# Kernel optimization log

Hardware: AMD Instinct MI355X
Metric: run time of the kernel (lower is better)

Reference implementation:

```python
import jax, jax.numpy as jnp
import numpy as np

C = 256          # channels
KS = 7           # kernel_size
G = 256          # groups (defaults to channels)
HID = C // 4     # hidden = channels // reduction
BN_EPS = 1e-5


def setup_inputs() -> dict:
    key = jax.random.key(0)
    ks = jax.random.split(key, 4)
    B, H, W = 4, 64, 64
    return {
        "x": jax.random.normal(ks[0], (B, C, H, W), jnp.float32),
        "reduce_w": jax.random.normal(ks[1], (HID, C), jnp.float32) / np.float32(np.sqrt(C)),
        "bn_gamma": jnp.ones((HID,), jnp.float32),
        "bn_beta": jnp.zeros((HID,), jnp.float32),
        "bn_mean": jnp.zeros((HID,), jnp.float32),
        "bn_var": jnp.ones((HID,), jnp.float32),
        "kproj_w": jax.random.normal(ks[2], (KS * KS * G, HID), jnp.float32) / np.float32(np.sqrt(HID)),
        "kproj_b": jnp.zeros((KS * KS * G,), jnp.float32),
    }


def _kernels(x, reduce_w, bn_gamma, bn_beta, bn_mean, bn_var, kproj_w, kproj_b):
    # 1x1 conv -> BN (eval mode) -> ReLU -> 1x1 conv, then per-pixel L2 kernel norm
    B, _, H, W = x.shape
    h = jnp.einsum('bchw,oc->bohw', x, reduce_w)
    inv = bn_gamma / jnp.sqrt(bn_var + BN_EPS)
    h = h * inv[None, :, None, None] + (bn_beta - bn_mean * inv)[None, :, None, None]
    h = jax.nn.relu(h)
    ker = jnp.einsum('bchw,oc->bohw', h, kproj_w) + kproj_b[None, :, None, None]
    ker = ker.reshape(B, G, KS * KS, H, W)           # (B, G, k*k, H, W)
    # kernel_norm == 'l2': zero-mean + unit L2 norm over the k*k taps
    ker = ker - ker.mean(axis=2, keepdims=True)
    denom = jnp.maximum(jnp.sqrt(jnp.sum(ker * ker, axis=2, keepdims=True)), 1e-6)
    return ker / denom


def reference(x, reduce_w, bn_gamma, bn_beta, bn_mean, bn_var, kproj_w, kproj_b):
    # get_kernels is under @torch.no_grad() in the original -> stop_gradient
    ker = jax.lax.stop_gradient(
        _kernels(x, reduce_w, bn_gamma, bn_beta, bn_mean, bn_var, kproj_w, kproj_b))
    B, Cc, H, W = x.shape
    pad = KS // 2
    gc = Cc // G  # = 1 for depthwise involution
    xp = jnp.pad(x, ((0, 0), (0, 0), (pad, pad), (pad, pad)))
    xg = xp.reshape(B, G, gc, H + 2 * pad, W + 2 * pad)
    # fused unfold-multiply-accumulate over the k*k taps (no (B,C,k,k,H,W) tensor)
    out = jnp.zeros((B, G, gc, H, W), x.dtype)
    for t in range(KS * KS):
        i, j = divmod(t, KS)
        out = out + xg[:, :, :, i:i + H, j:j + W] * ker[:, :, t][:, :, None]
    return out.reshape(B, Cc, H, W)
```

## Files before the change

### kernel.cpp

```cpp
#include <hip/hip_runtime.h>


#define C_    256
#define HID_  64
#define KS_   7
#define KK_   49
#define G_    256
#define H_    64
#define W_    64
#define HW_   4096
#define BN_EPS 1e-5f

typedef __attribute__((ext_vector_type(8))) short bf16x8;
typedef __attribute__((ext_vector_type(4))) float f32x4;

__device__ __forceinline__ ushort f2bf(float f) {
    unsigned u = __float_as_uint(f);
    return (ushort)((u + 0x7fffu + ((u >> 16) & 1u)) >> 16);
}
__device__ __forceinline__ float bf2f(ushort s) {
    return __uint_as_float((unsigned)s << 16);
}

__global__ __launch_bounds__(256) void prep_kernel(
    const float* __restrict__ kw, const float* __restrict__ kb,
    const float* __restrict__ reduce_w,
    const float* __restrict__ bn_gamma, const float* __restrict__ bn_beta,
    const float* __restrict__ bn_mean, const float* __restrict__ bn_var,
    ushort* __restrict__ kwb, float* __restrict__ rwT, float* __restrict__ betp,
    float* __restrict__ kbp)
{
    const int bid = blockIdx.x;
    if (bid < 256) {
        int idx  = bid * 256 + threadIdx.x;
        int base = idx * 16;
        int g    = base >> 12;
        int rem  = base & 4095;
        int t    = rem >> 6;
        int k0   = rem & 63;
        if (t == 49 || t == 50) return;
        union { ushort s[16]; uint4 v[2]; } u;
        if (t < KK_) {
            const float* src = kw + ((size_t)(g * KK_ + t)) * HID_ + k0;
            #pragma unroll
            for (int i = 0; i < 16; ++i) u.s[i] = f2bf(src[i]);
        } else {
            #pragma unroll
            for (int i = 0; i < 16; ++i) u.s[i] = 0;
        }
        uint4* dst = (uint4*)(kwb + base);
        dst[0] = u.v[0];
        dst[1] = u.v[1];
    } else if (bid == 256) {
        int k = threadIdx.x;
        #pragma unroll 1
        for (int o = 0; o < HID_; ++o) {
            float inv = bn_gamma[o] * rsqrtf(bn_var[o] + BN_EPS);
            rwT[k * HID_ + o] = reduce_w[o * C_ + k] * inv;
        }
        if (k < HID_) {
            float inv = bn_gamma[k] * rsqrtf(bn_var[k] + BN_EPS);
            betp[k] = bn_beta[k] - bn_mean[k] * inv;
        }
    } else if (bid == 257) {
        for (int i = threadIdx.x; i < G_ * 64; i += 256) {
            int g = i >> 6, t = i & 63;
            if (t == 49) continue;
            kbp[i] = (t < KK_) ? kb[g * KK_ + t] : 0.f;
        }
    } else {
        const int g = bid - 258;
        __shared__ float part[4][64];
        const int k  = threadIdx.x & 63;
        const int pr = threadIdx.x >> 6;
        const int t0 = pr * 13;
        const int t1 = (t0 + 13 < KK_) ? t0 + 13 : KK_;
        float s = 0.f;
        for (int t = t0; t < t1; ++t)
            s += kw[((size_t)(g * KK_ + t)) * HID_ + k];
        part[pr][k] = s;
        __syncthreads();
        if (threadIdx.x < 64) {
            float u = part[0][k] + part[1][k] + part[2][k] + part[3][k];
            ushort uh = f2bf(u);
            ushort ul = f2bf(u - bf2f(uh));
            kwb[(size_t)g * 4096 + 49 * 64 + k] = uh;
            kwb[(size_t)g * 4096 + 50 * 64 + k] = ul;
            float bs = (k < KK_) ? kb[g * KK_ + k] : 0.f;
            #pragma unroll
            for (int off = 32; off >= 1; off >>= 1) bs += __shfl_xor(bs, off);
            if (k == 0) kbp[g * 64 + 49] = bs;
        }
    }
}

__global__ __launch_bounds__(256) void hv1_kernel(
    const float* __restrict__ x, const float* __restrict__ rwT,
    float* __restrict__ hvp, int npx)
{
    const int lane = threadIdx.x & 63;
    const int wq   = __builtin_amdgcn_readfirstlane(threadIdx.x >> 6);
    const int kq   = blockIdx.y;
    const int p    = blockIdx.x * 64 + lane;
    const int b    = p >> 12;
    const int hw   = p & 4095;

    float acc[16];
    #pragma unroll
    for (int j = 0; j < 16; ++j) acc[j] = 0.f;

    const float* xp = x + ((size_t)b * C_ + kq * 64) * HW_ + hw;
    const float* rw = rwT + (kq * 64) * HID_ + wq * 16;
    #pragma unroll 8
    for (int kk = 0; kk < 64; ++kk) {
        float xk = xp[(size_t)kk * HW_];
        #pragma unroll
        for (int j = 0; j < 16; ++j) acc[j] = fmaf(xk, rw[kk * HID_ + j], acc[j]);
    }
    float* dst = hvp + ((size_t)(kq * 64 + wq * 16)) * npx + p;
    #pragma unroll
    for (int j = 0; j < 16; ++j) dst[(size_t)j * npx] = acc[j];
}

__global__ __launch_bounds__(256) void hv2_kernel(
    const float* __restrict__ hvp, const float* __restrict__ betp,
    ushort* __restrict__ hv, int npx)
{
    const int p  = blockIdx.x * 256 + threadIdx.x;
    const int o0 = blockIdx.y * 4;
    ushort s[4];
    #pragma unroll
    for (int j = 0; j < 4; ++j) {
        float v = 0.f;
        #pragma unroll
        for (int kq = 0; kq < 4; ++kq)
            v += hvp[(size_t)(kq * 64 + o0 + j) * npx + p];
        s[j] = f2bf(fmaxf(v + betp[o0 + j], 0.f));
    }
    uint2 w;
    w.x = (uint)s[0] | ((uint)s[1] << 16);
    w.y = (uint)s[2] | ((uint)s[3] << 16);
    *(uint2*)(hv + (size_t)p * HID_ + o0) = w;
}

__global__ __launch_bounds__(256) void invol_main(
    const float* __restrict__ x, const ushort* __restrict__ hv,
    const ushort* __restrict__ kwb, const float* __restrict__ kbp,
    float* __restrict__ out)
{
    __shared__ float x_s[38][72];
    __shared__ float hs_s[38][64];
    __shared__ float vs_s[32][64];

    const int tid  = threadIdx.x;
    const int lane = tid & 63;
    const int wave = __builtin_amdgcn_readfirstlane(tid >> 6);
    const int bg   = blockIdx.x;
    const int b    = bg >> 8;
    const int g    = bg & 255;
    const int y0   = blockIdx.y << 5;
    const int l15  = lane & 15;
    const int l4   = lane >> 4;

    const float* xg = x + (size_t)bg * HW_;
    for (int idx = tid; idx < 38 * 72; idx += 256) {
        int r = idx / 72, c = idx - r * 72;
        int yy = y0 - 3 + r;
        int cc = c - 3;
        bool v = ((unsigned)yy < 64u) && ((unsigned)cc < 64u);
        x_s[r][c] = v ? xg[yy * 64 + cc] : 0.f;
    }

    bf16x8 ka[2][4];
    const char* kwg = (const char*)kwb + (size_t)g * 8192;
    #pragma unroll
    for (int ks = 0; ks < 2; ++ks)
        #pragma unroll
        for (int tm = 0; tm < 4; ++tm) {
            int byte = (tm * 16 + l15) * 128 + ks * 64 + l4 * 16;
            ka[ks][tm] = *(const bf16x8*)(kwg + byte);
        }
    f32x4 kv[4];
    #pragma unroll
    for (int tm = 0; tm < 4; ++tm)
        kv[tm] = *(const f32x4*)(kbp + g * 64 + tm * 16 + l4 * 4);

    int po[3][4];
    #pragma unroll
    for (int tm = 0; tm < 3; ++tm)
        #pragma unroll
        for (int r = 0; r < 4; ++r) {
            int t = tm * 16 + l4 * 4 + r;
            int i = (t * 147) >> 10;
            int j = t - i * 7;
            po[tm][r] = i * 72 + l15 + j;
        }
    const int po48 = 6 * 72 + l15 + 6;

    __syncthreads();

    if (tid < 152) {
        int r  = tid >> 2;
        int c0 = (tid & 3) << 4;
        float s = 0.f;
        #pragma unroll
        for (int j = 0; j < 7; ++j) s += x_s[r][c0 + j];
        hs_s[r][c0] = s;
        #pragma unroll
        for (int c = 1; c < 16; ++c) {
            s += x_s[r][c0 + c + 6] - x_s[r][c0 + c - 1];
            hs_s[r][c0 + c] = s;
        }
    }
    __syncthreads();
    {
        int c   = tid & 63;
        int ry0 = (tid >> 6) << 3;
        float s = 0.f;
        #pragma unroll
        for (int i = 0; i < 7; ++i) s += hs_s[ry0 + i][c];
        vs_s[ry0][c] = s;
        #pragma unroll
        for (int k = 1; k < 8; ++k) {
            s += hs_s[ry0 + k + 6][c] - hs_s[ry0 + k - 1][c];
            vs_s[ry0 + k][c] = s;
        }
    }
    __syncthreads();

    const int rowpix0 = (b << 12) + (y0 << 6);

    #pragma unroll 2
    for (int rr = 0; rr < 8; ++rr) {
        const int ry = rr * 4 + wave;
        const int y  = y0 + ry;

        bf16x8 hb[2][4];
        #pragma unroll
        for (int ks = 0; ks < 2; ++ks)
            #pragma unroll
            for (int pn = 0; pn < 4; ++pn) {
                const char* p = (const char*)(hv +
                    (size_t)(rowpix0 + (ry << 6) + pn * 16 + l15) * HID_)
                    + ks * 64 + l4 * 16;
                hb[ks][pn] = *(const bf16x8*)p;
            }

        f32x4 acc[4][4];
        #pragma unroll
        for (int tm = 0; tm < 4; ++tm)
            #pragma unroll
            for (int pn = 0; pn < 4; ++pn) acc[tm][pn] = kv[tm];
        #pragma unroll
        for (int ks = 0; ks < 2; ++ks)
            #pragma unroll
            for (int tm = 0; tm < 4; ++tm)
                #pragma unroll
                for (int pn = 0; pn < 4; ++pn)
                    acc[tm][pn] = __builtin_amdgcn_mfma_f32_16x16x32_bf16(
                        ka[ks][tm], hb[ks][pn], acc[tm][pn], 0, 0, 0);

        float m_all[4], inv_[4];
        #pragma unroll
        for (int pn = 0; pn < 4; ++pn) {
            float ssq = 0.f;
            #pragma unroll
            for (int tm = 0; tm < 3; ++tm)
                #pragma unroll
                for (int r = 0; r < 4; ++r) {
                    float e = acc[tm][pn][r];
                    ssq = fmaf(e, e, ssq);
                }
            float e48 = acc[3][pn][0];
            ssq = fmaf(e48, e48, ssq);
            ssq += __shfl_xor(ssq, 16);
            ssq += __shfl_xor(ssq, 32);
            float mr = acc[3][pn][1] + acc[3][pn][2];
            float m  = __shfl(mr, l15) * (1.f / 49.f);
            float ss = fmaxf(ssq - 49.f * m * m, 0.f);
            m_all[pn] = m;
            inv_[pn]  = 1.f / fmaxf(sqrtf(ss), 1e-6f);
        }

        float kx[4] = {0.f, 0.f, 0.f, 0.f};
        const float* xrow = &x_s[ry][0];
        #pragma unroll
        for (int tm = 0; tm < 3; ++tm)
            #pragma unroll
            for (int r = 0; r < 4; ++r) {
                const float* bp = xrow + po[tm][r];
                #pragma unroll
                for (int pn = 0; pn < 4; ++pn)
                    kx[pn] = fmaf(acc[tm][pn][r], bp[pn * 16], kx[pn]);
            }
        {
            const float* bp = xrow + po48;
            #pragma unroll
            for (int pn = 0; pn < 4; ++pn)
                kx[pn] = fmaf(acc[3][pn][0], bp[pn * 16], kx[pn]);
        }
        float k2[4];
        #pragma unroll
        for (int pn = 0; pn < 4; ++pn) {
            float v = kx[pn];
            v += __shfl_xor(v, 16);
            v += __shfl_xor(v, 32);
            k2[pn] = v;
        }
        float k2s = (l4 == 0) ? k2[0] : (l4 == 1) ? k2[1] : (l4 == 2) ? k2[2] : k2[3];
        float ms  = (l4 == 0) ? m_all[0] : (l4 == 1) ? m_all[1] : (l4 == 2) ? m_all[2] : m_all[3];
        float is  = (l4 == 0) ? inv_[0] : (l4 == 1) ? inv_[1] : (l4 == 2) ? inv_[2] : inv_[3];
        float x2  = vs_s[ry][lane];
        out[(size_t)bg * HW_ + (y << 6) + lane] = (k2s - ms * x2) * is;
    }
}

__global__ __launch_bounds__(256) void hv_kernel(
    const float* __restrict__ x, const float* __restrict__ rwT,
    const float* __restrict__ betp, ushort* __restrict__ hv)
{
    const int lane = threadIdx.x & 63;
    const int q    = __builtin_amdgcn_readfirstlane(threadIdx.x >> 6);
    const int p    = blockIdx.x * 64 + lane;
    const int b    = p >> 12;
    const int hw   = p & 4095;
    float acc[16];
    #pragma unroll
    for (int j = 0; j < 16; ++j) acc[j] = betp[q * 16 + j];
    const float* xp = x + (size_t)b * C_ * HW_ + hw;
    #pragma unroll 8
    for (int k = 0; k < C_; ++k) {
        float xk = xp[(size_t)k * HW_];
        const float* rw = rwT + k * HID_ + q * 16;
        #pragma unroll
        for (int j = 0; j < 16; ++j) acc[j] = fmaf(xk, rw[j], acc[j]);
    }
    union { ushort s[16]; uint4 v[2]; } u;
    #pragma unroll
    for (int j = 0; j < 16; ++j) u.s[j] = f2bf(fmaxf(acc[j], 0.f));
    uint4* dst = (uint4*)(hv + (size_t)p * HID_ + q * 16);
    dst[0] = u.v[0];
    dst[1] = u.v[1];
}

__global__ __launch_bounds__(256) void invol_fallback(
    const float* __restrict__ x, const float* __restrict__ reduce_w,
    const float* __restrict__ bn_gamma, const float* __restrict__ bn_beta,
    const float* __restrict__ bn_mean, const float* __restrict__ bn_var,
    const float* __restrict__ kw, const float* __restrict__ kb,
    float* __restrict__ out)
{
    __shared__ float rwT[C_][HID_ + 4];
    __shared__ float bns[HID_];
    __shared__ float bnb[HID_];
    const int tid = threadIdx.x;
    const int b  = blockIdx.z;
    const int g0 = blockIdx.y * 32;
    const int p  = blockIdx.x * 256 + tid;
    const int py = p >> 6;
    const int px = p & 63;
    #pragma unroll 1
    for (int o = 0; o < HID_; ++o) rwT[tid][o] = reduce_w[o * C_ + tid];
    if (tid < HID_) {
        float inv = bn_gamma[tid] * rsqrtf(bn_var[tid] + BN_EPS);
        bns[tid] = inv;
        bnb[tid] = bn_beta[tid] - bn_mean[tid] * inv;
    }
    __syncthreads();
    float hvv[HID_];
    #pragma unroll
    for (int o = 0; o < HID_; ++o) hvv[o] = 0.f;
    const float* xb = x + (size_t)b * C_ * HW_ + p;
    #pragma unroll 4
    for (int k = 0; k < C_; ++k) {
        float xk = xb[(size_t)k * HW_];
        const float4* wr = (const float4*)&rwT[k][0];
        #pragma unroll
        for (int o4 = 0; o4 < HID_ / 4; ++o4) {
            float4 w = wr[o4];
            hvv[o4*4+0] = fmaf(xk, w.x, hvv[o4*4+0]);
            hvv[o4*4+1] = fmaf(xk, w.y, hvv[o4*4+1]);
            hvv[o4*4+2] = fmaf(xk, w.z, hvv[o4*4+2]);
            hvv[o4*4+3] = fmaf(xk, w.w, hvv[o4*4+3]);
        }
    }
    #pragma unroll
    for (int o = 0; o < HID_; ++o) hvv[o] = fmaxf(fmaf(hvv[o], bns[o], bnb[o]), 0.f);
    #pragma unroll 1
    for (int gi = 0; gi < 32; ++gi) {
        const int g = g0 + gi;
        const float* kwg = kw + (size_t)g * KK_ * HID_;
        float acc[KK_];
        #pragma unroll
        for (int t = 0; t < KK_; ++t) {
            float a = kb[g * KK_ + t];
            const float4* row = (const float4*)(kwg + t * HID_);
            #pragma unroll
            for (int k4 = 0; k4 < HID_ / 4; ++k4) {
                float4 w = row[k4];
                a = fmaf(w.x, hvv[k4*4+0], a);
                a = fmaf(w.y, hvv[k4*4+1], a);
                a = fmaf(w.z, hvv[k4*4+2], a);
                a = fmaf(w.w, hvv[k4*4+3], a);
            }
            acc[t] = a;
        }
        float mean = 0.f;
        #pragma unroll
        for (int t = 0; t < KK_; ++t) mean += acc[t];
        mean *= (1.f / 49.f);
        float ss = 0.f;
        #pragma unroll
        for (int t = 0; t < KK_; ++t) { acc[t] -= mean; ss = fmaf(acc[t], acc[t], ss); }
        float inv = 1.f / fmaxf(sqrtf(ss), 1e-6f);
        const float* xg = x + ((size_t)(b * G_ + g)) * HW_;
        float oacc = 0.f;
        #pragma unroll
        for (int i = 0; i < KS_; ++i) {
            int yv = py + i - 3;
            bool rok = ((unsigned)yv < (unsigned)H_);
            const float* xrow = xg + yv * W_;
            #pragma unroll
            for (int j = 0; j < KS_; ++j) {
                int xx = px + j - 3;
                bool ok = rok && ((unsigned)xx < (unsigned)W_);
                float v = ok ? xrow[xx] : 0.f;
                oacc = fmaf(v, acc[i*7+j], oacc);
            }
        }
        out[((size_t)(b * G_ + g)) * HW_ + p] = oacc * inv;
    }
}

extern "C" void kernel_launch(void* const* d_in, const int* in_sizes, int n_in,
                              void* d_out, int out_size, void* d_ws, size_t ws_size,
                              hipStream_t stream) {
    const float* x        = (const float*)d_in[0];
    const float* reduce_w = (const float*)d_in[1];
    const float* bn_gamma = (const float*)d_in[2];
    const float* bn_beta  = (const float*)d_in[3];
    const float* bn_mean  = (const float*)d_in[4];
    const float* bn_var   = (const float*)d_in[5];
    const float* kproj_w  = (const float*)d_in[6];
    const float* kproj_b  = (const float*)d_in[7];
    float* out = (float*)d_out;
    const int B   = in_sizes[0] / (C_ * HW_);
    const int npx = B * HW_;

    size_t kwb_off = 0;
    size_t kwb_sz  = (size_t)G_ * 64 * 64 * 2;
    size_t kbp_off = kwb_off + kwb_sz;
    size_t kbp_sz  = (size_t)G_ * 64 * 4;
    size_t rwt_off = kbp_off + kbp_sz;
    size_t rwt_sz  = (size_t)C_ * HID_ * 4;
    size_t bet_off = rwt_off + rwt_sz;
    size_t bet_sz  = 256;
    size_t hv_off  = bet_off + bet_sz;
    size_t hv_sz   = (size_t)npx * HID_ * 2;
    size_t hvp_off = hv_off + hv_sz;
    size_t hvp_sz  = (size_t)4 * HID_ * npx * 4;
    size_t need2   = hvp_off;
    size_t need    = hvp_off + hvp_sz;

    if (ws_size < need2) {
        dim3 grid(HW_ / 256, G_ / 32, B);
        invol_fallback<<<grid, 256, 0, stream>>>(x, reduce_w, bn_gamma, bn_beta,
                                                 bn_mean, bn_var, kproj_w, kproj_b, out);
        return;
    }

    ushort* kwb  = (ushort*)((char*)d_ws + kwb_off);
    float*  kbp  = (float*)((char*)d_ws + kbp_off);
    float*  rwT  = (float*)((char*)d_ws + rwt_off);
    float*  betp = (float*)((char*)d_ws + bet_off);
    ushort* hv   = (ushort*)((char*)d_ws + hv_off);
    float*  hvp  = (float*)((char*)d_ws + hvp_off);

    prep_kernel<<<dim3(258 + G_), 256, 0, stream>>>(kproj_w, kproj_b, reduce_w,
                                                    bn_gamma, bn_beta, bn_mean, bn_var,
                                                    kwb, rwT, betp, kbp);
    if (ws_size >= need) {
        hv1_kernel<<<dim3(npx / 64, 4), 256, 0, stream>>>(x, rwT, hvp, npx);
        hv2_kernel<<<dim3(npx / 256, 16), 256, 0, stream>>>(hvp, betp, hv, npx);
    } else {
        hv_kernel<<<dim3(npx / 64), 256, 0, stream>>>(x, rwT, betp, hv);
    }
    invol_main<<<dim3(B * G_, 2), 256, 0, stream>>>(x, hv, kwb, kbp, out);
}
```

Baseline: 148.8 us.

## Double-buffer hv loads, replicate mean taps, and merge cross-lane reductions

The main loop in the involution kernel now uses two register buffers for the bf16 hidden vectors, so loads for the next row pair are issued while the current rows run their MFMAs and epilogue. The sum-row weights and bias are replicated into all four padded tap slots, so every lane group holds the mean term without the extra __shfl broadcast. The per-pixel sum-of-squares and kx reductions use a select-and-exchange pattern that needs fewer shuffles. The box-sum prologue caches shared-memory values in registers. This raises register pressure and leaves more code written as macros.

Result: slower. 154.7 us, median of 2 (+4.0%).

```diff
diff --git a/kernel.cpp b/kernel.cpp
--- a/kernel.cpp
+++ b/kernel.cpp
@@ -20,6 +20,20 @@
 }
 __device__ __forceinline__ float bf2f(ushort s) {
     return __uint_as_float((unsigned)s << 16);
+}
+__device__ __forceinline__ float sel4(int l4, float a0, float a1, float a2, float a3) {
+    float lo = (l4 & 1) ? a1 : a0;
+    float hi = (l4 & 1) ? a3 : a2;
+    return (l4 & 2) ? hi : lo;
+}
+__device__ __forceinline__ float reduce4(int l4, float v0, float v1, float v2, float v3) {
+    float own = sel4(l4, v0, v1, v2, v3);
+    float x1  = sel4(l4, v1, v0, v3, v2);
+    float x2_ = sel4(l4, v2, v3, v0, v1);
+    float x3  = sel4(l4, v3, v2, v1, v0);
+    float s1  = own + __shfl_xor(x1, 16);
+    float s1c = x2_ + __shfl_xor(x3, 16);
+    return s1 + __shfl_xor(s1c, 32);
 }
 
 __global__ __launch_bounds__(256) void prep_kernel(
@@ -38,7 +52,7 @@
         int rem  = base & 4095;
         int t    = rem >> 6;
         int k0   = rem & 63;
-        if (t == 49 || t == 50) return;
+        if (t >= 49 && ((t - 49) & 3) <= 1) return;
         union { ushort s[16]; uint4 v[2]; } u;
         if (t < KK_) {
             const float* src = kw + ((size_t)(g * KK_ + t)) * HID_ + k0;
@@ -65,7 +79,7 @@
     } else if (bid == 257) {
         for (int i = threadIdx.x; i < G_ * 64; i += 256) {
             int g = i >> 6, t = i & 63;
-            if (t == 49) continue;
+            if (t >= 49 && ((t - 49) & 3) == 0) continue;
             kbp[i] = (t < KK_) ? kb[g * KK_ + t] : 0.f;
         }
     } else {
@@ -84,12 +98,18 @@
             float u = part[0][k] + part[1][k] + part[2][k] + part[3][k];
             ushort uh = f2bf(u);
             ushort ul = f2bf(u - bf2f(uh));
-            kwb[(size_t)g * 4096 + 49 * 64 + k] = uh;
-            kwb[(size_t)g * 4096 + 50 * 64 + k] = ul;
+            #pragma unroll
+            for (int rr = 0; rr < 4; ++rr) {
+                kwb[(size_t)g * 4096 + (49 + rr * 4) * 64 + k] = uh;
+                kwb[(size_t)g * 4096 + (50 + rr * 4) * 64 + k] = ul;
+            }
             float bs = (k < KK_) ? kb[g * KK_ + k] : 0.f;
             #pragma unroll
             for (int off = 32; off >= 1; off >>= 1) bs += __shfl_xor(bs, off);
-            if (k == 0) kbp[g * 64 + 49] = bs;
+            if (k == 0) {
+                #pragma unroll
+                for (int rr = 0; rr < 4; ++rr) kbp[g * 64 + 49 + rr * 4] = bs;
+            }
         }
     }
 }
@@ -202,13 +222,14 @@
     if (tid < 152) {
         int r  = tid >> 2;
         int c0 = (tid & 3) << 4;
-        float s = 0.f;
-        #pragma unroll
-        for (int j = 0; j < 7; ++j) s += x_s[r][c0 + j];
+        float v[22];
+        #pragma unroll
+        for (int i = 0; i < 22; ++i) v[i] = x_s[r][c0 + i];
+        float s = v[0] + v[1] + v[2] + v[3] + v[4] + v[5] + v[6];
         hs_s[r][c0] = s;
         #pragma unroll
         for (int c = 1; c < 16; ++c) {
-            s += x_s[r][c0 + c + 6] - x_s[r][c0 + c - 1];
+            s += v[c + 6] - v[c - 1];
             hs_s[r][c0 + c] = s;
         }
     }
@@ -216,13 +237,14 @@
     {
         int c   = tid & 63;
         int ry0 = (tid >> 6) << 3;
-        float s = 0.f;
-        #pragma unroll
-        for (int i = 0; i < 7; ++i) s += hs_s[ry0 + i][c];
+        float h[14];
+        #pragma unroll
+        for (int i = 0; i < 14; ++i) h[i] = hs_s[ry0 + i][c];
+        float s = h[0] + h[1] + h[2] + h[3] + h[4] + h[5] + h[6];
         vs_s[ry0][c] = s;
         #pragma unroll
         for (int k = 1; k < 8; ++k) {
-            s += hs_s[ry0 + k + 6][c] - hs_s[ry0 + k - 1][c];
+            s += h[k + 6] - h[k - 1];
             vs_s[ry0 + k][c] = s;
         }
     }
@@ -230,89 +252,89 @@
 
     const int rowpix0 = (b << 12) + (y0 << 6);
 
-    #pragma unroll 2
-    for (int rr = 0; rr < 8; ++rr) {
-        const int ry = rr * 4 + wave;
-        const int y  = y0 + ry;
-
-        bf16x8 hb[2][4];
-        #pragma unroll
-        for (int ks = 0; ks < 2; ++ks)
-            #pragma unroll
-            for (int pn = 0; pn < 4; ++pn) {
-                const char* p = (const char*)(hv +
-                    (size_t)(rowpix0 + (ry << 6) + pn * 16 + l15) * HID_)
-                    + ks * 64 + l4 * 16;
-                hb[ks][pn] = *(const bf16x8*)p;
-            }
-
-        f32x4 acc[4][4];
-        #pragma unroll
-        for (int tm = 0; tm < 4; ++tm)
-            #pragma unroll
-            for (int pn = 0; pn < 4; ++pn) acc[tm][pn] = kv[tm];
-        #pragma unroll
-        for (int ks = 0; ks < 2; ++ks)
-            #pragma unroll
-            for (int tm = 0; tm < 4; ++tm)
-                #pragma unroll
-                for (int pn = 0; pn < 4; ++pn)
-                    acc[tm][pn] = __builtin_amdgcn_mfma_f32_16x16x32_bf16(
-                        ka[ks][tm], hb[ks][pn], acc[tm][pn], 0, 0, 0);
-
-        float m_all[4], inv_[4];
-        #pragma unroll
-        for (int pn = 0; pn < 4; ++pn) {
-            float ssq = 0.f;
-            #pragma unroll
-            for (int tm = 0; tm < 3; ++tm)
-                #pragma unroll
-                for (int r = 0; r < 4; ++r) {
-                    float e = acc[tm][pn][r];
-                    ssq = fmaf(e, e, ssq);
-                }
-            float e48 = acc[3][pn][0];
-            ssq = fmaf(e48, e48, ssq);
-            ssq += __shfl_xor(ssq, 16);
-            ssq += __shfl_xor(ssq, 32);
-            float mr = acc[3][pn][1] + acc[3][pn][2];
-            float m  = __shfl(mr, l15) * (1.f / 49.f);
-            float ss = fmaxf(ssq - 49.f * m * m, 0.f);
-            m_all[pn] = m;
-            inv_[pn]  = 1.f / fmaxf(sqrtf(ss), 1e-6f);
-        }
-
-        float kx[4] = {0.f, 0.f, 0.f, 0.f};
-        const float* xrow = &x_s[ry][0];
-        #pragma unroll
-        for (int tm = 0; tm < 3; ++tm)
-            #pragma unroll
-            for (int r = 0; r < 4; ++r) {
-                const float* bp = xrow + po[tm][r];
-                #pragma unroll
-                for (int pn = 0; pn < 4; ++pn)
-                    kx[pn] = fmaf(acc[tm][pn][r], bp[pn * 16], kx[pn]);
-            }
-        {
-            const float* bp = xrow + po48;
-            #pragma unroll
-            for (int pn = 0; pn < 4; ++pn)
-                kx[pn] = fmaf(acc[3][pn][0], bp[pn * 16], kx[pn]);
-        }
-        float k2[4];
-        #pragma unroll
-        for (int pn = 0; pn < 4; ++pn) {
-            float v = kx[pn];
-            v += __shfl_xor(v, 16);
-            v += __shfl_xor(v, 32);
-            k2[pn] = v;
-        }
-        float k2s = (l4 == 0) ? k2[0] : (l4 == 1) ? k2[1] : (l4 == 2) ? k2[2] : k2[3];
-        float ms  = (l4 == 0) ? m_all[0] : (l4 == 1) ? m_all[1] : (l4 == 2) ? m_all[2] : m_all[3];
-        float is  = (l4 == 0) ? inv_[0] : (l4 == 1) ? inv_[1] : (l4 == 2) ? inv_[2] : inv_[3];
-        float x2  = vs_s[ry][lane];
-        out[(size_t)bg * HW_ + (y << 6) + lane] = (k2s - ms * x2) * is;
-    }
+#define LOAD_HB(HB, RY) do {                                               \
+    const int ryl_ = (RY);                                                 \
+    _Pragma("unroll")                                                      \
+    for (int ks = 0; ks < 2; ++ks)                                         \
+        _Pragma("unroll")                                                  \
+        for (int pn = 0; pn < 4; ++pn) {                                   \
+            const char* p_ = (const char*)(hv +                            \
+                (size_t)(rowpix0 + (ryl_ << 6) + pn * 16 + l15) * HID_)    \
+                + ks * 64 + l4 * 16;                                       \
+            HB[ks][pn] = *(const bf16x8*)p_;                               \
+        }                                                                  \
+} while (0)
+
+#define BODY(HB, RY) do {                                                  \
+    const int ry_ = (RY);                                                  \
+    f32x4 acc[4][4];                                                       \
+    _Pragma("unroll")                                                      \
+    for (int tm = 0; tm < 4; ++tm)                                         \
+        _Pragma("unroll")                                                  \
+        for (int pn = 0; pn < 4; ++pn) acc[tm][pn] = kv[tm];               \
+    _Pragma("unroll")                                                      \
+    for (int ks = 0; ks < 2; ++ks)                                         \
+        _Pragma("unroll")                                                  \
+        for (int tm = 0; tm < 4; ++tm)                                     \
+            _Pragma("unroll")                                              \
+            for (int pn = 0; pn < 4; ++pn)                                 \
+                acc[tm][pn] = __builtin_amdgcn_mfma_f32_16x16x32_bf16(     \
+                    ka[ks][tm], HB[ks][pn], acc[tm][pn], 0, 0, 0);         \
+    float ssqp[4], mp[4], kxp[4];                                          \
+    const float* xrow = &x_s[ry_][0];                                      \
+    _Pragma("unroll")                                                      \
+    for (int pn = 0; pn < 4; ++pn) {                                       \
+        float ssq = 0.f;                                                   \
+        _Pragma("unroll")                                                  \
+        for (int tm = 0; tm < 3; ++tm)                                     \
+            _Pragma("unroll")                                              \
+            for (int r = 0; r < 4; ++r) {                                  \
+                float e = acc[tm][pn][r];                                  \
+                ssq = fmaf(e, e, ssq);                                     \
+            }                                                              \
+        float e48 = acc[3][pn][0];                                         \
+        ssqp[pn] = fmaf(e48, e48, ssq);                                    \
+        mp[pn] = (acc[3][pn][1] + acc[3][pn][2]) * (1.f / 49.f);           \
+        kxp[pn] = 0.f;                                                     \
+    }                                                                      \
+    _Pragma("unroll")                                                      \
+    for (int tm = 0; tm < 3; ++tm)                                         \
+        _Pragma("unroll")                                                  \
+        for (int r = 0; r < 4; ++r) {                                      \
+            const float* bp = xrow + po[tm][r];                            \
+            _Pragma("unroll")                                              \
+            for (int pn = 0; pn < 4; ++pn)                                 \
+                kxp[pn] = fmaf(acc[tm][pn][r], bp[pn * 16], kxp[pn]);      \
+        }                                                                  \
+    {                                                                      \
+        const float* bp = xrow + po48;                                     \
+        _Pragma("unroll")                                                  \
+        for (int pn = 0; pn < 4; ++pn)                                     \
+            kxp[pn] = fmaf(acc[3][pn][0], bp[pn * 16], kxp[pn]);           \
+    }                                                                      \
+    float kxo = reduce4(l4, kxp[0], kxp[1], kxp[2], kxp[3]);               \
+    float sso = reduce4(l4, ssqp[0], ssqp[1], ssqp[2], ssqp[3]);           \
+    float mo  = sel4(l4, mp[0], mp[1], mp[2], mp[3]);                      \
+    float ss  = fmaxf(sso - 49.f * mo * mo, 0.f);                          \
+    float is  = 1.f / fmaxf(sqrtf(ss), 1e-6f);                             \
+    float x2  = vs_s[ry_][lane];                                           \
+    out[(size_t)bg * HW_ + ((y0 + ry_) << 6) + lane] = (kxo - mo * x2) * is; \
+} while (0)
+
+    bf16x8 hbA[2][4], hbB[2][4];
+    LOAD_HB(hbA, wave);
+    LOAD_HB(hbB, 4 + wave);
+    #pragma unroll 1
+    for (int rr2 = 0; rr2 < 3; ++rr2) {
+        BODY(hbA, rr2 * 8 + wave);
+        LOAD_HB(hbA, rr2 * 8 + 8 + wave);
+        BODY(hbB, rr2 * 8 + 4 + wave);
+        LOAD_HB(hbB, rr2 * 8 + 12 + wave);
+    }
+    BODY(hbA, 24 + wave);
+    BODY(hbB, 28 + wave);
+#undef LOAD_HB
+#undef BODY
 }
 
 __global__ __launch_bounds__(256) void hv_kernel(
```

## Replace per-pixel shuffle reductions with transposed permlane-swap reduction in involution epilogue

Applied to the files above, without the earlier changes.

The epilogue replaces eight shfl_xor cross-lane reductions plus a broadcast shuffle per row with a transposed 4-way reduction built on permlane16/32 swap builtins, so each lane finishes only its own pixel. To avoid the mean broadcast shuffle, the sum-row weights are replicated into every 16-row tm=3 slot in the prepacked weights and biases. The vertical box-sum pass and its barrier and LDS buffer are removed; the vertical sum is computed inline from the horizontal sums. The horizontal pass also caches its row in registers. This trades extra selects and a few extra LDS reads per row for fewer cross-lane ops and one less sync.

Result: slower. 197.7 us (median of 2 runs) (+32.9%).

```diff
diff --git a/kernel.cpp b/kernel.cpp
--- a/kernel.cpp
+++ b/kernel.cpp
@@ -13,6 +13,7 @@
 
 typedef __attribute__((ext_vector_type(8))) short bf16x8;
 typedef __attribute__((ext_vector_type(4))) float f32x4;
+typedef __attribute__((ext_vector_type(2))) unsigned uv2;
 
 __device__ __forceinline__ ushort f2bf(float f) {
     unsigned u = __float_as_uint(f);
@@ -20,6 +21,38 @@
 }
 __device__ __forceinline__ float bf2f(ushort s) {
     return __uint_as_float((unsigned)s << 16);
+}
+__device__ __forceinline__ float sel4(int l4, float a0, float a1, float a2, float a3) {
+    float lo = (l4 & 1) ? a1 : a0;
+    float hi = (l4 & 1) ? a3 : a2;
+    return (l4 & 2) ? hi : lo;
+}
+__device__ __forceinline__ float xor16p(float v) {
+#if __has_builtin(__builtin_amdgcn_permlane16_swap)
+    uv2 r = __builtin_amdgcn_permlane16_swap(__float_as_uint(v), __float_as_uint(v),
+                                             false, false);
+    return (__uint_as_float(r[0]) + __uint_as_float(r[1])) - v;
+#else
+    return __shfl_xor(v, 16);
+#endif
+}
+__device__ __forceinline__ float xor32p(float v) {
+#if __has_builtin(__builtin_amdgcn_permlane32_swap)
+    uv2 r = __builtin_amdgcn_permlane32_swap(__float_as_uint(v), __float_as_uint(v),
+                                             false, false);
+    return (__uint_as_float(r[0]) + __uint_as_float(r[1])) - v;
+#else
+    return __shfl_xor(v, 32);
+#endif
+}
+__device__ __forceinline__ float reduce4(int l4, float v0, float v1, float v2, float v3) {
+    float own = sel4(l4, v0, v1, v2, v3);
+    float x1  = sel4(l4, v1, v0, v3, v2);
+    float x2_ = sel4(l4, v2, v3, v0, v1);
+    float x3  = sel4(l4, v3, v2, v1, v0);
+    float s1  = own + xor16p(x1);
+    float s1c = x2_ + xor16p(x3);
+    return s1 + xor32p(s1c);
 }
 
 __global__ __launch_bounds__(256) void prep_kernel(
@@ -38,7 +71,7 @@
         int rem  = base & 4095;
         int t    = rem >> 6;
         int k0   = rem & 63;
-        if (t == 49 || t == 50) return;
+        if (t >= 49 && ((t - 49) & 3) <= 1) return;
         union { ushort s[16]; uint4 v[2]; } u;
         if (t < KK_) {
             const float* src = kw + ((size_t)(g * KK_ + t)) * HID_ + k0;
@@ -65,7 +98,7 @@
     } else if (bid == 257) {
         for (int i = threadIdx.x; i < G_ * 64; i += 256) {
             int g = i >> 6, t = i & 63;
-            if (t == 49) continue;
+            if (t >= 49 && ((t - 49) & 3) == 0) continue;
             kbp[i] = (t < KK_) ? kb[g * KK_ + t] : 0.f;
         }
     } else {
@@ -84,12 +117,18 @@
             float u = part[0][k] + part[1][k] + part[2][k] + part[3][k];
             ushort uh = f2bf(u);
             ushort ul = f2bf(u - bf2f(uh));
-            kwb[(size_t)g * 4096 + 49 * 64 + k] = uh;
-            kwb[(size_t)g * 4096 + 50 * 64 + k] = ul;
+            #pragma unroll
+            for (int rr = 0; rr < 4; ++rr) {
+                kwb[(size_t)g * 4096 + (49 + rr * 4) * 64 + k] = uh;
+                kwb[(size_t)g * 4096 + (50 + rr * 4) * 64 + k] = ul;
+            }
             float bs = (k < KK_) ? kb[g * KK_ + k] : 0.f;
             #pragma unroll
             for (int off = 32; off >= 1; off >>= 1) bs += __shfl_xor(bs, off);
-            if (k == 0) kbp[g * 64 + 49] = bs;
+            if (k == 0) {
+                #pragma unroll
+                for (int rr = 0; rr < 4; ++rr) kbp[g * 64 + 49 + rr * 4] = bs;
+            }
         }
     }
 }
@@ -150,7 +189,6 @@
 {
     __shared__ float x_s[38][72];
     __shared__ float hs_s[38][64];
-    __shared__ float vs_s[32][64];
 
     const int tid  = threadIdx.x;
     const int lane = tid & 63;
@@ -202,28 +240,15 @@
     if (tid < 152) {
         int r  = tid >> 2;
         int c0 = (tid & 3) << 4;
-        float s = 0.f;
-        #pragma unroll
-        for (int j = 0; j < 7; ++j) s += x_s[r][c0 + j];
+        float v[22];
+        #pragma unroll
+        for (int i = 0; i < 22; ++i) v[i] = x_s[r][c0 + i];
+        float s = v[0] + v[1] + v[2] + v[3] + v[4] + v[5] + v[6];
         hs_s[r][c0] = s;
         #pragma unroll
         for (int c = 1; c < 16; ++c) {
-            s += x_s[r][c0 + c + 6] - x_s[r][c0 + c - 1];
+            s += v[c + 6] - v[c - 1];
             hs_s[r][c0 + c] = s;
-        }
-    }
-    __syncthreads();
-    {
-        int c   = tid & 63;
-        int ry0 = (tid >> 6) << 3;
-        float s = 0.f;
-        #pragma unroll
-        for (int i = 0; i < 7; ++i) s += hs_s[ry0 + i][c];
-        vs_s[ry0][c] = s;
-        #pragma unroll
-        for (int k = 1; k < 8; ++k) {
-            s += hs_s[ry0 + k + 6][c] - hs_s[ry0 + k - 1][c];
-            vs_s[ry0 + k][c] = s;
         }
     }
     __syncthreads();
@@ -233,7 +258,6 @@
     #pragma unroll 2
     for (int rr = 0; rr < 8; ++rr) {
         const int ry = rr * 4 + wave;
-        const int y  = y0 + ry;
 
         bf16x8 hb[2][4];
         #pragma unroll
@@ -246,6 +270,10 @@
                 hb[ks][pn] = *(const bf16x8*)p;
             }
 
+        float x2 = hs_s[ry][lane] + hs_s[ry + 1][lane] + hs_s[ry + 2][lane]
+                 + hs_s[ry + 3][lane] + hs_s[ry + 4][lane]
+                 + hs_s[ry + 5][lane] + hs_s[ry + 6][lane];
+
         f32x4 acc[4][4];
         #pragma unroll
         for (int tm = 0; tm < 4; ++tm)
@@ -260,7 +288,8 @@
                     acc[tm][pn] = __builtin_amdgcn_mfma_f32_16x16x32_bf16(
                         ka[ks][tm], hb[ks][pn], acc[tm][pn], 0, 0, 0);
 
-        float m_all[4], inv_[4];
+        float ssqp[4], mp[4], kxp[4];
+        const float* xrow = &x_s[ry][0];
         #pragma unroll
         for (int pn = 0; pn < 4; ++pn) {
             float ssq = 0.f;
@@ -272,18 +301,10 @@
                     ssq = fmaf(e, e, ssq);
                 }
             float e48 = acc[3][pn][0];
-            ssq = fmaf(e48, e48, ssq);
-            ssq += __shfl_xor(ssq, 16);
-            ssq += __shfl_xor(ssq, 32);
-            float mr = acc[3][pn][1] + acc[3][pn][2];
-            float m  = __shfl(mr, l15) * (1.f / 49.f);
-            float ss = fmaxf(ssq - 49.f * m * m, 0.f);
-            m_all[pn] = m;
-            inv_[pn]  = 1.f / fmaxf(sqrtf(ss), 1e-6f);
-        }
-
-        float kx[4] = {0.f, 0.f, 0.f, 0.f};
-        const float* xrow = &x_s[ry][0];
+            ssqp[pn] = fmaf(e48, e48, ssq);
+            mp[pn]  = (acc[3][pn][1] + acc[3][pn][2]) * (1.f / 49.f);
+            kxp[pn] = 0.f;
+        }
         #pragma unroll
         for (int tm = 0; tm < 3; ++tm)
             #pragma unroll
@@ -291,27 +312,21 @@
                 const float* bp = xrow + po[tm][r];
                 #pragma unroll
                 for (int pn = 0; pn < 4; ++pn)
-                    kx[pn] = fmaf(acc[tm][pn][r], bp[pn * 16], kx[pn]);
+                    kxp[pn] = fmaf(acc[tm][pn][r], bp[pn * 16], kxp[pn]);
             }
         {
             const float* bp = xrow + po48;
             #pragma unroll
             for (int pn = 0; pn < 4; ++pn)
-                kx[pn] = fmaf(acc[3][pn][0], bp[pn * 16], kx[pn]);
-        }
-        float k2[4];
-        #pragma unroll
-        for (int pn = 0; pn < 4; ++pn) {
-            float v = kx[pn];
-            v += __shfl_xor(v, 16);
-            v += __shfl_xor(v, 32);
-            k2[pn] = v;
-        }
-        float k2s = (l4 == 0) ? k2[0] : (l4 == 1) ? k2[1] : (l4 == 2) ? k2[2] : k2[3];
-        float ms  = (l4 == 0) ? m_all[0] : (l4 == 1) ? m_all[1] : (l4 == 2) ? m_all[2] : m_all[3];
-        float is  = (l4 == 0) ? inv_[0] : (l4 == 1) ? inv_[1] : (l4 == 2) ? inv_[2] : inv_[3];
-        float x2  = vs_s[ry][lane];
-        out[(size_t)bg * HW_ + (y << 6) + lane] = (k2s - ms * x2) * is;
+                kxp[pn] = fmaf(acc[3][pn][0], bp[pn * 16], kxp[pn]);
+        }
+
+        float kxo = reduce4(l4, kxp[0], kxp[1], kxp[2], kxp[3]);
+        float sso = reduce4(l4, ssqp[0], ssqp[1], ssqp[2], ssqp[3]);
+        float mo  = sel4(l4, mp[0], mp[1], mp[2], mp[3]);
+        float ss  = fmaxf(sso - 49.f * mo * mo, 0.f);
+        float is  = 1.f / fmaxf(sqrtf(ss), 1e-6f);
+        out[(size_t)bg * HW_ + ((y0 + ry) << 6) + lane] = (kxo - mo * x2) * is;
     }
 }
 
```
